# Kernel tuning notes

Hardware: AMD Instinct MI355X
Metric: run time of the kernel (lower is better)

## Reference

```python
import jax, jax.numpy as jnp
import numpy as np

B, N = 2, 65536
C_DIM, HID, OUT_DIM = 128, 32, 1
Z = Y = X = 64
SLOPE = 0.01  # torch default leaky_relu negative slope
TOTAL_PARAMS = 3 * HID + HID + HID * HID + HID + HID * OUT_DIM + OUT_DIM  # 1217


def leaky(x):
    return jnp.where(x >= 0, x, SLOPE * x)


def sample_grid_feature(c, p):
    """Trilinear grid_sample, align_corners=True, border padding.
    c: [B, C, Z, Y, X]; p: [B, N, 3] with (x, y, z) voxel coords -> [B, N, C]."""
    Bc, C, Zc, Yc, Xc = c.shape
    cb = jnp.moveaxis(c, 1, -1)  # [B, Z, Y, X, C]

    def src_index(v, S):
        # normalize_gridcloud -> clamp(-2,2) -> grid_sample unnormalize -> border clip
        g = jnp.clip(2.0 * v / (S - 1) - 1.0, -2.0, 2.0)
        ix = (g + 1.0) * 0.5 * (S - 1)
        return jnp.clip(ix, 0.0, S - 1)  # border padding clips the coordinate

    ix = src_index(p[..., 0], Xc)
    iy = src_index(p[..., 1], Yc)
    iz = src_index(p[..., 2], Zc)

    x0 = jnp.floor(ix); y0 = jnp.floor(iy); z0 = jnp.floor(iz)
    wx = ix - x0; wy = iy - y0; wz = iz - z0
    x0i = jnp.clip(x0.astype(jnp.int32), 0, Xc - 1); x1i = jnp.clip(x0i + 1, 0, Xc - 1)
    y0i = jnp.clip(y0.astype(jnp.int32), 0, Yc - 1); y1i = jnp.clip(y0i + 1, 0, Yc - 1)
    z0i = jnp.clip(z0.astype(jnp.int32), 0, Zc - 1); z1i = jnp.clip(z0i + 1, 0, Zc - 1)

    bidx = jnp.arange(Bc)[:, None]  # [B,1] broadcasts with [B,N] indices

    def g(zi, yi, xi):
        return cb[bidx, zi, yi, xi]  # [B, N, C]

    wx = wx[..., None]; wy = wy[..., None]; wz = wz[..., None]
    c00 = g(z0i, y0i, x0i) * (1 - wx) + g(z0i, y0i, x1i) * wx
    c01 = g(z0i, y1i, x0i) * (1 - wx) + g(z0i, y1i, x1i) * wx
    c10 = g(z1i, y0i, x0i) * (1 - wx) + g(z1i, y0i, x1i) * wx
    c11 = g(z1i, y1i, x0i) * (1 - wx) + g(z1i, y1i, x1i) * wx
    c0 = c00 * (1 - wy) + c01 * wy
    c1 = c10 * (1 - wy) + c11 * wy
    return c0 * (1 - wz) + c1 * wz


def setup_inputs() -> dict:
    key = jax.random.key(0)
    ks = jax.random.split(key, 8)
    pcl = jax.random.normal(ks[0], (B, N, 3), dtype=jnp.float32)
    pcl_mem = jax.random.uniform(ks[1], (B, N, 3), dtype=jnp.float32,
                                 minval=0.0, maxval=float(X - 1))
    c_plane = jax.random.normal(ks[2], (B, C_DIM, Z, Y, X), dtype=jnp.float32) * 0.1
    std = 0.21  # weights_init
    Wh1 = jax.random.normal(ks[3], (C_DIM, HID), dtype=jnp.float32) * std
    bh1 = jnp.zeros((HID,), jnp.float32)
    Wh2 = jax.random.normal(ks[4], (HID, HID), dtype=jnp.float32) * std
    bh2 = jnp.zeros((HID,), jnp.float32)
    Wh3 = jax.random.normal(ks[5], (HID, TOTAL_PARAMS), dtype=jnp.float32) * std
    bh3 = jnp.zeros((TOTAL_PARAMS,), jnp.float32)
    return {"pcl": pcl, "pcl_mem": pcl_mem, "c_plane": c_plane,
            "Wh1": Wh1, "bh1": bh1, "Wh2": Wh2, "bh2": bh2, "Wh3": Wh3, "bh3": bh3}


def reference(pcl, pcl_mem, c_plane, Wh1, bh1, Wh2, bh2, Wh3, bh3):
    feats = sample_grid_feature(c_plane, pcl_mem)  # [B, N, c_dim]
    # hypernet MLP producing per-point dynamic weights
    h = leaky(feats @ Wh1 + bh1)
    h = leaky(h @ Wh2 + bh2)
    hw = h @ Wh3 + bh3  # [B, N, 1217]

    p = 0
    W1 = hw[..., p:p + 3 * HID].reshape(B, N, 3, HID); p += 3 * HID
    b1 = hw[..., p:p + HID]; p += HID
    W2 = hw[..., p:p + HID * HID].reshape(B, N, HID, HID); p += HID * HID
    b2 = hw[..., p:p + HID]; p += HID
    W3 = hw[..., p:p + HID * OUT_DIM].reshape(B, N, HID, OUT_DIM); p += HID * OUT_DIM
    b3 = hw[..., p:p + OUT_DIM]

    # hyp.use_delta_mem_coords: fractional offset within voxel, centered
    x = pcl_mem - jnp.trunc(pcl_mem) - 0.5  # [B, N, 3]

    o = jnp.einsum('bni,bnio->bno', x, W1) + b1
    o = jnp.einsum('bni,bnio->bno', leaky(o), W2) + b2
    o = jnp.einsum('bni,bnio->bno', leaky(o), W3) + b3  # [B, N, 1]
    out = o[..., 0]  # squeeze(-1)
    return (out, feats)
```

## Files before the change

kernel.cpp:

```cpp
#include <hip/hip_runtime.h>
#include <cstdint>

#define NB 2
#define NPER 65536
#define NPTS (NB*NPER)
#define CDIM 128
#define SV 64
#define VOX (SV*SV*SV)
#define WCOLS 1217
#define WSTRIDE 1232

typedef float f2 __attribute__((ext_vector_type(2)));

__device__ __forceinline__ f2 mk2(float a, float b){ f2 r; r.x=a; r.y=b; return r; }
__device__ __forceinline__ f2 pkfma(f2 a, f2 b, f2 c){
#if __has_builtin(__builtin_elementwise_fma)
    return __builtin_elementwise_fma(a, b, c);
#else
    f2 r; r.x = fmaf(a.x, b.x, c.x); r.y = fmaf(a.y, b.y, c.y); return r;
#endif
}

__global__ __launch_bounds__(256) void transpose_kernel(const float* __restrict__ in,
                                                        float* __restrict__ out){
    __shared__ float tile[128][33];
    const int blk = blockIdx.x;
    const int b  = blk >> 13;
    const int v0 = (blk & 8191) << 5;
    const int tx = threadIdx.x & 31;
    const int ty = threadIdx.x >> 5;
    const float* ip = in + (size_t)b*128*VOX + v0;
    #pragma unroll
    for (int cc = 0; cc < 16; cc++){
        int c = cc*8 + ty;
        tile[c][tx] = ip[(size_t)c*VOX + tx];
    }
    __syncthreads();
    const int cx = threadIdx.x & 127;
    const int vy = threadIdx.x >> 7;
    float* op = out + ((size_t)b*VOX + v0)*128;
    #pragma unroll
    for (int vv = 0; vv < 16; vv++){
        int v = vv*2 + vy;
        op[(size_t)v*128 + cx] = tile[cx][v];
    }
}

__global__ __launch_bounds__(256) void sample_kernel(const float* __restrict__ pcl_mem,
                                                     const float* __restrict__ ct,
                                                     float* __restrict__ feats){
    const int tid  = threadIdx.x;
    const int lane = tid & 63;
    const int p    = blockIdx.x*4 + (tid >> 6);
    const int b    = p >> 16;

    float v0 = pcl_mem[3*p+0], v1 = pcl_mem[3*p+1], v2 = pcl_mem[3*p+2];
    auto src = [](float v){
        float g = 2.0f*v/63.0f - 1.0f;
        g = fminf(fmaxf(g, -2.0f), 2.0f);
        float t = (g + 1.0f)*0.5f*63.0f;
        return fminf(fmaxf(t, 0.0f), 63.0f);
    };
    float ix = src(v0), iy = src(v1), iz = src(v2);
    float fx = floorf(ix), fy = floorf(iy), fz = floorf(iz);
    float wx = ix-fx, wy = iy-fy, wz = iz-fz;
    int x0 = min(max((int)fx,0),63); int x1 = min(x0+1,63);
    int y0 = min(max((int)fy,0),63); int y1 = min(y0+1,63);
    int z0 = min(max((int)fz,0),63); int z1 = min(z0+1,63);
    float wx0 = 1.f-wx, wy0 = 1.f-wy, wz0 = 1.f-wz;

    const float2* base = (const float2*)ct + (size_t)b*VOX*64 + lane;
    float ax = 0.f, ay = 0.f;
#define CORNER(zz,yy,xx,wgt) { \
        float2 cv = base[(size_t)(((zz)*64+(yy))*64+(xx))*64]; \
        float w_ = (wgt); \
        ax = fmaf(w_, cv.x, ax); ay = fmaf(w_, cv.y, ay); }
    CORNER(z0,y0,x0, wz0*wy0*wx0);
    CORNER(z0,y0,x1, wz0*wy0*wx );
    CORNER(z0,y1,x0, wz0*wy *wx0);
    CORNER(z0,y1,x1, wz0*wy *wx );
    CORNER(z1,y0,x0, wz *wy0*wx0);
    CORNER(z1,y0,x1, wz *wy0*wx );
    CORNER(z1,y1,x0, wz *wy *wx0);
    CORNER(z1,y1,x1, wz *wy *wx );
#undef CORNER
    ((float2*)(feats + (size_t)p*CDIM))[lane] = make_float2(ax, ay);
}

__global__ __launch_bounds__(256) void sample_slow_kernel(const float* __restrict__ pcl_mem,
                                                          const float* __restrict__ cpl,
                                                          float* __restrict__ feats){
    int gid = blockIdx.x*256 + threadIdx.x;
    int p = gid >> 7; int c = gid & 127;
    int b = p >> 16;
    float v0 = pcl_mem[3*p+0], v1 = pcl_mem[3*p+1], v2 = pcl_mem[3*p+2];
    auto src = [](float v){
        float g = 2.0f*v/63.0f - 1.0f;
        g = fminf(fmaxf(g, -2.0f), 2.0f);
        float t = (g + 1.0f)*0.5f*63.0f;
        return fminf(fmaxf(t, 0.0f), 63.0f);
    };
    float ix = src(v0), iy = src(v1), iz = src(v2);
    float fx = floorf(ix), fy = floorf(iy), fz = floorf(iz);
    float wx = ix-fx, wy = iy-fy, wz = iz-fz;
    int x0 = min(max((int)fx,0),63); int x1 = min(x0+1,63);
    int y0 = min(max((int)fy,0),63); int y1 = min(y0+1,63);
    int z0 = min(max((int)fz,0),63); int z1 = min(z0+1,63);
    float wx0 = 1.f-wx, wy0 = 1.f-wy, wz0 = 1.f-wz;
    const float* base = cpl + ((size_t)(b*128 + c))*VOX;
    float acc = 0.f;
    acc = fmaf(wz0*wy0*wx0, base[(z0*64+y0)*64+x0], acc);
    acc = fmaf(wz0*wy0*wx , base[(z0*64+y0)*64+x1], acc);
    acc = fmaf(wz0*wy *wx0, base[(z0*64+y1)*64+x0], acc);
    acc = fmaf(wz0*wy *wx , base[(z0*64+y1)*64+x1], acc);
    acc = fmaf(wz *wy0*wx0, base[(z1*64+y0)*64+x0], acc);
    acc = fmaf(wz *wy0*wx , base[(z1*64+y0)*64+x1], acc);
    acc = fmaf(wz *wy *wx0, base[(z1*64+y1)*64+x0], acc);
    acc = fmaf(wz *wy *wx , base[(z1*64+y1)*64+x1], acc);
    feats[gid] = acc;
}

__global__ __launch_bounds__(512) void mlp_kernel(
        const float* __restrict__ pcl_mem,
        const float* __restrict__ Wh1, const float* __restrict__ bh1,
        const float* __restrict__ Wh2, const float* __restrict__ bh2,
        const float* __restrict__ Wh3, const float* __restrict__ bh3,
        const float* __restrict__ feats,
        float* __restrict__ outp)
{
    __shared__ __align__(16) float W3s[32*WSTRIDE];
    const int tid = threadIdx.x;
    const int p   = blockIdx.x*512 + tid;

    for (int t = tid; t < 32*WCOLS; t += 512){
        int k = t / WCOLS;
        int c = t - k*WCOLS;
        W3s[k*WSTRIDE + c] = Wh3[t];
    }
    __syncthreads();

    float xv0, xv1, xv2;
    {
        float v0 = pcl_mem[3*p+0], v1 = pcl_mem[3*p+1], v2 = pcl_mem[3*p+2];
        xv0 = v0 - truncf(v0) - 0.5f;
        xv1 = v1 - truncf(v1) - 0.5f;
        xv2 = v2 - truncf(v2) - 0.5f;
    }

    const float4* f4  = (const float4*)(feats + (size_t)p*CDIM);
    const float4* W1q = (const float4*)Wh1;
    const float4* W2q = (const float4*)Wh2;
    const float4* b1q = (const float4*)bh1;
    const float4* b2q = (const float4*)bh2;
    const float4* b3q = (const float4*)bh3;

    f2 h1v[16];
    #pragma unroll
    for (int jv=0;jv<8;jv++){ float4 bv=b1q[jv]; h1v[2*jv]=mk2(bv.x,bv.y); h1v[2*jv+1]=mk2(bv.z,bv.w); }
    for (int c4=0;c4<32;c4++){
        float4 f = f4[c4];
        float fs[4] = {f.x, f.y, f.z, f.w};
        #pragma unroll
        for (int cc=0;cc<4;cc++){
            f2 fc = mk2(fs[cc], fs[cc]);
            #pragma unroll
            for (int jv=0;jv<8;jv++){
                float4 w = W1q[(c4*4+cc)*8 + jv];
                h1v[2*jv]   = pkfma(fc, mk2(w.x,w.y), h1v[2*jv]);
                h1v[2*jv+1] = pkfma(fc, mk2(w.z,w.w), h1v[2*jv+1]);
            }
        }
    }
    float ha[32];
    #pragma unroll
    for (int t=0;t<16;t++){
        float a0=h1v[t].x, a1=h1v[t].y;
        ha[2*t]   = fmaxf(a0, 0.01f*a0);
        ha[2*t+1] = fmaxf(a1, 0.01f*a1);
    }

    f2 h2v[16];
    #pragma unroll
    for (int kv=0;kv<8;kv++){ float4 bv=b2q[kv]; h2v[2*kv]=mk2(bv.x,bv.y); h2v[2*kv+1]=mk2(bv.z,bv.w); }
    #pragma unroll
    for (int j=0;j<32;j++){
        f2 aj = mk2(ha[j], ha[j]);
        #pragma unroll
        for (int kv=0;kv<8;kv++){
            float4 w = W2q[j*8+kv];
            h2v[2*kv]   = pkfma(aj, mk2(w.x,w.y), h2v[2*kv]);
            h2v[2*kv+1] = pkfma(aj, mk2(w.z,w.w), h2v[2*kv+1]);
        }
    }
    float h2a[32];
    #pragma unroll
    for (int t=0;t<16;t++){
        float a0=h2v[t].x, a1=h2v[t].y;
        h2a[2*t]   = fmaxf(a0, 0.01f*a0);
        h2a[2*t+1] = fmaxf(a1, 0.01f*a1);
    }

    const f2 x0 = mk2(xv0,xv0), x1 = mk2(xv1,xv1), x2 = mk2(xv2,xv2);

    float a1r[32];
    #pragma unroll
    for (int jc=0;jc<4;jc++){
        f2 accv[4];
        #pragma unroll
        for (int q=0;q<2;q++){
            float4 ba=b3q[jc*2+q], bb=b3q[8+jc*2+q], bc=b3q[16+jc*2+q], bd=b3q[24+jc*2+q];
            accv[2*q]   = pkfma(x0,mk2(ba.x,ba.y), pkfma(x1,mk2(bb.x,bb.y), pkfma(x2,mk2(bc.x,bc.y), mk2(bd.x,bd.y))));
            accv[2*q+1] = pkfma(x0,mk2(ba.z,ba.w), pkfma(x1,mk2(bb.z,bb.w), pkfma(x2,mk2(bc.z,bc.w), mk2(bd.z,bd.w))));
        }
        #pragma unroll
        for (int k=0;k<32;k++){
            const float4* row = (const float4*)(W3s + k*WSTRIDE) + jc*2;
            f2 hk = mk2(h2a[k], h2a[k]);
            #pragma unroll
            for (int q=0;q<2;q++){
                float4 wa=row[q], wb=row[8+q], wc=row[16+q], wd=row[24+q];
                f2 m0 = pkfma(x0,mk2(wa.x,wa.y), pkfma(x1,mk2(wb.x,wb.y), pkfma(x2,mk2(wc.x,wc.y), mk2(wd.x,wd.y))));
                f2 m1 = pkfma(x0,mk2(wa.z,wa.w), pkfma(x1,mk2(wb.z,wb.w), pkfma(x2,mk2(wc.z,wc.w), mk2(wd.z,wd.w))));
                accv[2*q]   = pkfma(hk, m0, accv[2*q]);
                accv[2*q+1] = pkfma(hk, m1, accv[2*q+1]);
            }
        }
        #pragma unroll
        for (int q=0;q<2;q++){
            float a0=accv[2*q].x, a1=accv[2*q].y, a2=accv[2*q+1].x, a3=accv[2*q+1].y;
            a1r[jc*8+4*q+0] = fmaxf(a0, 0.01f*a0);
            a1r[jc*8+4*q+1] = fmaxf(a1, 0.01f*a1);
            a1r[jc*8+4*q+2] = fmaxf(a2, 0.01f*a2);
            a1r[jc*8+4*q+3] = fmaxf(a3, 0.01f*a3);
        }
    }

    f2 o2v[16];
    #pragma unroll
    for (int jv=0;jv<8;jv++){ float4 bv=b3q[288+jv]; o2v[2*jv]=mk2(bv.x,bv.y); o2v[2*jv+1]=mk2(bv.z,bv.w); }
    #pragma unroll
    for (int k=0;k<32;k++){
        const float4* row = (const float4*)(W3s + k*WSTRIDE) + 288;
        f2 hk = mk2(h2a[k], h2a[k]);
        #pragma unroll
        for (int jv=0;jv<8;jv++){
            float4 w = row[jv];
            o2v[2*jv]   = pkfma(hk, mk2(w.x,w.y), o2v[2*jv]);
            o2v[2*jv+1] = pkfma(hk, mk2(w.z,w.w), o2v[2*jv+1]);
        }
    }

    #pragma unroll 1
    for (int i=0;i<32;i++){
        f2 ai = mk2(a1r[0], a1r[0]);
        f2 w2v[16];
        #pragma unroll
        for (int jv=0;jv<8;jv++){ float4 bv=b3q[32+i*8+jv]; w2v[2*jv]=mk2(bv.x,bv.y); w2v[2*jv+1]=mk2(bv.z,bv.w); }
        #pragma unroll
        for (int k=0;k<32;k++){
            const float4* row = (const float4*)(W3s + k*WSTRIDE) + 32 + i*8;
            f2 hk = mk2(h2a[k], h2a[k]);
            #pragma unroll
            for (int jv=0;jv<8;jv++){
                float4 w = row[jv];
                w2v[2*jv]   = pkfma(hk, mk2(w.x,w.y), w2v[2*jv]);
                w2v[2*jv+1] = pkfma(hk, mk2(w.z,w.w), w2v[2*jv+1]);
            }
        }
        #pragma unroll
        for (int t=0;t<16;t++) o2v[t] = pkfma(ai, w2v[t], o2v[t]);
        #pragma unroll
        for (int t=0;t<31;t++) a1r[t] = a1r[t+1];
    }

    float a2r[32];
    #pragma unroll
    for (int t=0;t<16;t++){
        float a0=o2v[t].x, a1=o2v[t].y;
        a2r[2*t]   = fmaxf(a0, 0.01f*a0);
        a2r[2*t+1] = fmaxf(a1, 0.01f*a1);
    }

    float o3 = bh3[1216];
    #pragma unroll
    for (int k=0;k<32;k++) o3 = fmaf(h2a[k], W3s[k*WSTRIDE + 1216], o3);
    #pragma unroll
    for (int jc=0;jc<4;jc++){
        float w3c[8];
        #pragma unroll
        for (int q=0;q<2;q++){
            float4 bv=b3q[296+jc*2+q];
            w3c[4*q]=bv.x; w3c[4*q+1]=bv.y; w3c[4*q+2]=bv.z; w3c[4*q+3]=bv.w;
        }
        #pragma unroll
        for (int k=0;k<32;k++){
            const float4* row = (const float4*)(W3s + k*WSTRIDE) + 296 + jc*2;
            float hk = h2a[k];
            #pragma unroll
            for (int q=0;q<2;q++){
                float4 w=row[q];
                w3c[4*q+0] = fmaf(hk, w.x, w3c[4*q+0]);
                w3c[4*q+1] = fmaf(hk, w.y, w3c[4*q+1]);
                w3c[4*q+2] = fmaf(hk, w.z, w3c[4*q+2]);
                w3c[4*q+3] = fmaf(hk, w.w, w3c[4*q+3]);
            }
        }
        #pragma unroll
        for (int r=0;r<8;r++) o3 = fmaf(a2r[jc*8+r], w3c[r], o3);
    }

    outp[p] = o3;
}

extern "C" void kernel_launch(void* const* d_in, const int* in_sizes, int n_in,
                              void* d_out, int out_size, void* d_ws, size_t ws_size,
                              hipStream_t stream)
{
    const float* pcl_mem = (const float*)d_in[1];
    const float* c_plane = (const float*)d_in[2];
    const float* Wh1     = (const float*)d_in[3];
    const float* bh1     = (const float*)d_in[4];
    const float* Wh2     = (const float*)d_in[5];
    const float* bh2     = (const float*)d_in[6];
    const float* Wh3     = (const float*)d_in[7];
    const float* bh3     = (const float*)d_in[8];
    float* outp  = (float*)d_out;
    float* feats = outp + NPTS;

    const size_t ct_bytes = (size_t)NB*VOX*CDIM*sizeof(float);
    if (ws_size >= ct_bytes) {
        float* ct = (float*)d_ws;
        transpose_kernel<<<NB*(VOX/32), 256, 0, stream>>>(c_plane, ct);
        sample_kernel<<<NPTS/4, 256, 0, stream>>>(pcl_mem, ct, feats);
    } else {
        sample_slow_kernel<<<(NPTS*CDIM)/256, 256, 0, stream>>>(pcl_mem, c_plane, feats);
    }

    mlp_kernel<<<NPTS/512, 512, 0, stream>>>(pcl_mem, Wh1, bh1, Wh2, bh2, Wh3, bh3, feats, outp);
}
```

Before: 715.8 us.

## Process two points per thread in MLP kernel to reuse shared-memory weight loads

Each thread of the MLP kernel now computes two points, so each shared-memory read of the hypernet output weights feeds two sets of FMAs. The block shrinks to 256 threads with the same 512 points per block, and the W2-generation loop is split into column chunks to limit live registers. This targets LDS bandwidth as the limit in the per-point dynamic-weight stage. In exchange it roughly doubles register pressure and halves the threads per block, which may lower occupancy or cause spills.

```diff
diff --git a/kernel.cpp b/kernel.cpp
--- a/kernel.cpp
+++ b/kernel.cpp
@@ -120,7 +120,7 @@
     feats[gid] = acc;
 }
 
-__global__ __launch_bounds__(512) void mlp_kernel(
+__global__ __launch_bounds__(256, 1) void mlp_kernel(
         const float* __restrict__ pcl_mem,
         const float* __restrict__ Wh1, const float* __restrict__ bh1,
         const float* __restrict__ Wh2, const float* __restrict__ bh2,
@@ -130,186 +130,255 @@
 {
     __shared__ __align__(16) float W3s[32*WSTRIDE];
     const int tid = threadIdx.x;
-    const int p   = blockIdx.x*512 + tid;
-
-    for (int t = tid; t < 32*WCOLS; t += 512){
+    const int pA  = blockIdx.x*512 + tid;
+    const int pB  = pA + 256;
+
+    for (int t = tid; t < 32*WCOLS; t += 256){
         int k = t / WCOLS;
         int c = t - k*WCOLS;
         W3s[k*WSTRIDE + c] = Wh3[t];
     }
     __syncthreads();
 
-    float xv0, xv1, xv2;
+    float xA0, xA1, xA2, xB0, xB1, xB2;
     {
-        float v0 = pcl_mem[3*p+0], v1 = pcl_mem[3*p+1], v2 = pcl_mem[3*p+2];
-        xv0 = v0 - truncf(v0) - 0.5f;
-        xv1 = v1 - truncf(v1) - 0.5f;
-        xv2 = v2 - truncf(v2) - 0.5f;
-    }
-
-    const float4* f4  = (const float4*)(feats + (size_t)p*CDIM);
+        float v0 = pcl_mem[3*pA+0], v1 = pcl_mem[3*pA+1], v2 = pcl_mem[3*pA+2];
+        xA0 = v0 - truncf(v0) - 0.5f; xA1 = v1 - truncf(v1) - 0.5f; xA2 = v2 - truncf(v2) - 0.5f;
+        float u0 = pcl_mem[3*pB+0], u1 = pcl_mem[3*pB+1], u2 = pcl_mem[3*pB+2];
+        xB0 = u0 - truncf(u0) - 0.5f; xB1 = u1 - truncf(u1) - 0.5f; xB2 = u2 - truncf(u2) - 0.5f;
+    }
+
+    const float4* f4A = (const float4*)(feats + (size_t)pA*CDIM);
+    const float4* f4B = (const float4*)(feats + (size_t)pB*CDIM);
     const float4* W1q = (const float4*)Wh1;
     const float4* W2q = (const float4*)Wh2;
     const float4* b1q = (const float4*)bh1;
     const float4* b2q = (const float4*)bh2;
     const float4* b3q = (const float4*)bh3;
 
-    f2 h1v[16];
-    #pragma unroll
-    for (int jv=0;jv<8;jv++){ float4 bv=b1q[jv]; h1v[2*jv]=mk2(bv.x,bv.y); h1v[2*jv+1]=mk2(bv.z,bv.w); }
+    f2 h1A[16], h1B[16];
+    #pragma unroll
+    for (int jv=0;jv<8;jv++){
+        float4 bv=b1q[jv];
+        h1A[2*jv]=mk2(bv.x,bv.y); h1A[2*jv+1]=mk2(bv.z,bv.w);
+        h1B[2*jv]=mk2(bv.x,bv.y); h1B[2*jv+1]=mk2(bv.z,bv.w);
+    }
     for (int c4=0;c4<32;c4++){
-        float4 f = f4[c4];
-        float fs[4] = {f.x, f.y, f.z, f.w};
+        float4 fa = f4A[c4], fb = f4B[c4];
+        float fsA[4] = {fa.x, fa.y, fa.z, fa.w};
+        float fsB[4] = {fb.x, fb.y, fb.z, fb.w};
         #pragma unroll
         for (int cc=0;cc<4;cc++){
-            f2 fc = mk2(fs[cc], fs[cc]);
+            f2 fcA = mk2(fsA[cc], fsA[cc]);
+            f2 fcB = mk2(fsB[cc], fsB[cc]);
             #pragma unroll
             for (int jv=0;jv<8;jv++){
                 float4 w = W1q[(c4*4+cc)*8 + jv];
-                h1v[2*jv]   = pkfma(fc, mk2(w.x,w.y), h1v[2*jv]);
-                h1v[2*jv+1] = pkfma(fc, mk2(w.z,w.w), h1v[2*jv+1]);
-            }
-        }
-    }
-    float ha[32];
+                f2 wlo = mk2(w.x,w.y), whi = mk2(w.z,w.w);
+                h1A[2*jv]   = pkfma(fcA, wlo, h1A[2*jv]);
+                h1A[2*jv+1] = pkfma(fcA, whi, h1A[2*jv+1]);
+                h1B[2*jv]   = pkfma(fcB, wlo, h1B[2*jv]);
+                h1B[2*jv+1] = pkfma(fcB, whi, h1B[2*jv+1]);
+            }
+        }
+    }
+    float haA[32], haB[32];
     #pragma unroll
     for (int t=0;t<16;t++){
-        float a0=h1v[t].x, a1=h1v[t].y;
-        ha[2*t]   = fmaxf(a0, 0.01f*a0);
-        ha[2*t+1] = fmaxf(a1, 0.01f*a1);
-    }
-
-    f2 h2v[16];
-    #pragma unroll
-    for (int kv=0;kv<8;kv++){ float4 bv=b2q[kv]; h2v[2*kv]=mk2(bv.x,bv.y); h2v[2*kv+1]=mk2(bv.z,bv.w); }
+        float a0=h1A[t].x, a1=h1A[t].y, b0=h1B[t].x, b1=h1B[t].y;
+        haA[2*t]=fmaxf(a0,0.01f*a0); haA[2*t+1]=fmaxf(a1,0.01f*a1);
+        haB[2*t]=fmaxf(b0,0.01f*b0); haB[2*t+1]=fmaxf(b1,0.01f*b1);
+    }
+
+    f2 h2A[16], h2B[16];
+    #pragma unroll
+    for (int kv=0;kv<8;kv++){
+        float4 bv=b2q[kv];
+        h2A[2*kv]=mk2(bv.x,bv.y); h2A[2*kv+1]=mk2(bv.z,bv.w);
+        h2B[2*kv]=mk2(bv.x,bv.y); h2B[2*kv+1]=mk2(bv.z,bv.w);
+    }
     #pragma unroll
     for (int j=0;j<32;j++){
-        f2 aj = mk2(ha[j], ha[j]);
+        f2 ajA = mk2(haA[j], haA[j]);
+        f2 ajB = mk2(haB[j], haB[j]);
         #pragma unroll
         for (int kv=0;kv<8;kv++){
             float4 w = W2q[j*8+kv];
-            h2v[2*kv]   = pkfma(aj, mk2(w.x,w.y), h2v[2*kv]);
-            h2v[2*kv+1] = pkfma(aj, mk2(w.z,w.w), h2v[2*kv+1]);
-        }
-    }
-    float h2a[32];
+            f2 wlo = mk2(w.x,w.y), whi = mk2(w.z,w.w);
+            h2A[2*kv]   = pkfma(ajA, wlo, h2A[2*kv]);
+            h2A[2*kv+1] = pkfma(ajA, whi, h2A[2*kv+1]);
+            h2B[2*kv]   = pkfma(ajB, wlo, h2B[2*kv]);
+            h2B[2*kv+1] = pkfma(ajB, whi, h2B[2*kv+1]);
+        }
+    }
+    float h2aA[32], h2aB[32];
     #pragma unroll
     for (int t=0;t<16;t++){
-        float a0=h2v[t].x, a1=h2v[t].y;
-        h2a[2*t]   = fmaxf(a0, 0.01f*a0);
-        h2a[2*t+1] = fmaxf(a1, 0.01f*a1);
-    }
-
-    const f2 x0 = mk2(xv0,xv0), x1 = mk2(xv1,xv1), x2 = mk2(xv2,xv2);
-
-    float a1r[32];
+        float a0=h2A[t].x, a1=h2A[t].y, b0=h2B[t].x, b1=h2B[t].y;
+        h2aA[2*t]=fmaxf(a0,0.01f*a0); h2aA[2*t+1]=fmaxf(a1,0.01f*a1);
+        h2aB[2*t]=fmaxf(b0,0.01f*b0); h2aB[2*t+1]=fmaxf(b1,0.01f*b1);
+    }
+
+    const f2 xa0=mk2(xA0,xA0), xa1=mk2(xA1,xA1), xa2=mk2(xA2,xA2);
+    const f2 xb0=mk2(xB0,xB0), xb1=mk2(xB1,xB1), xb2=mk2(xB2,xB2);
+
+    float a1A[32], a1B[32];
     #pragma unroll
     for (int jc=0;jc<4;jc++){
-        f2 accv[4];
+        f2 accA[4], accB[4];
         #pragma unroll
         for (int q=0;q<2;q++){
             float4 ba=b3q[jc*2+q], bb=b3q[8+jc*2+q], bc=b3q[16+jc*2+q], bd=b3q[24+jc*2+q];
-            accv[2*q]   = pkfma(x0,mk2(ba.x,ba.y), pkfma(x1,mk2(bb.x,bb.y), pkfma(x2,mk2(bc.x,bc.y), mk2(bd.x,bd.y))));
-            accv[2*q+1] = pkfma(x0,mk2(ba.z,ba.w), pkfma(x1,mk2(bb.z,bb.w), pkfma(x2,mk2(bc.z,bc.w), mk2(bd.z,bd.w))));
+            f2 balo=mk2(ba.x,ba.y), bahi=mk2(ba.z,ba.w);
+            f2 bblo=mk2(bb.x,bb.y), bbhi=mk2(bb.z,bb.w);
+            f2 bclo=mk2(bc.x,bc.y), bchi=mk2(bc.z,bc.w);
+            f2 bdlo=mk2(bd.x,bd.y), bdhi=mk2(bd.z,bd.w);
+            accA[2*q]   = pkfma(xa0,balo, pkfma(xa1,bblo, pkfma(xa2,bclo, bdlo)));
+            accA[2*q+1] = pkfma(xa0,bahi, pkfma(xa1,bbhi, pkfma(xa2,bchi, bdhi)));
+            accB[2*q]   = pkfma(xb0,balo, pkfma(xb1,bblo, pkfma(xb2,bclo, bdlo)));
+            accB[2*q+1] = pkfma(xb0,bahi, pkfma(xb1,bbhi, pkfma(xb2,bchi, bdhi)));
         }
         #pragma unroll
         for (int k=0;k<32;k++){
             const float4* row = (const float4*)(W3s + k*WSTRIDE) + jc*2;
-            f2 hk = mk2(h2a[k], h2a[k]);
+            f2 hkA = mk2(h2aA[k], h2aA[k]);
+            f2 hkB = mk2(h2aB[k], h2aB[k]);
             #pragma unroll
             for (int q=0;q<2;q++){
                 float4 wa=row[q], wb=row[8+q], wc=row[16+q], wd=row[24+q];
-                f2 m0 = pkfma(x0,mk2(wa.x,wa.y), pkfma(x1,mk2(wb.x,wb.y), pkfma(x2,mk2(wc.x,wc.y), mk2(wd.x,wd.y))));
-                f2 m1 = pkfma(x0,mk2(wa.z,wa.w), pkfma(x1,mk2(wb.z,wb.w), pkfma(x2,mk2(wc.z,wc.w), mk2(wd.z,wd.w))));
-                accv[2*q]   = pkfma(hk, m0, accv[2*q]);
-                accv[2*q+1] = pkfma(hk, m1, accv[2*q+1]);
+                f2 walo=mk2(wa.x,wa.y), wahi=mk2(wa.z,wa.w);
+                f2 wblo=mk2(wb.x,wb.y), wbhi=mk2(wb.z,wb.w);
+                f2 wclo=mk2(wc.x,wc.y), wchi=mk2(wc.z,wc.w);
+                f2 wdlo=mk2(wd.x,wd.y), wdhi=mk2(wd.z,wd.w);
+                f2 mA0 = pkfma(xa0,walo, pkfma(xa1,wblo, pkfma(xa2,wclo, wdlo)));
+                f2 mA1 = pkfma(xa0,wahi, pkfma(xa1,wbhi, pkfma(xa2,wchi, wdhi)));
+                f2 mB0 = pkfma(xb0,walo, pkfma(xb1,wblo, pkfma(xb2,wclo, wdlo)));
+                f2 mB1 = pkfma(xb0,wahi, pkfma(xb1,wbhi, pkfma(xb2,wchi, wdhi)));
+                accA[2*q]   = pkfma(hkA, mA0, accA[2*q]);
+                accA[2*q+1] = pkfma(hkA, mA1, accA[2*q+1]);
+                accB[2*q]   = pkfma(hkB, mB0, accB[2*q]);
+                accB[2*q+1] = pkfma(hkB, mB1, accB[2*q+1]);
             }
         }
         #pragma unroll
         for (int q=0;q<2;q++){
-            float a0=accv[2*q].x, a1=accv[2*q].y, a2=accv[2*q+1].x, a3=accv[2*q+1].y;
-            a1r[jc*8+4*q+0] = fmaxf(a0, 0.01f*a0);
-            a1r[jc*8+4*q+1] = fmaxf(a1, 0.01f*a1);
-            a1r[jc*8+4*q+2] = fmaxf(a2, 0.01f*a2);
-            a1r[jc*8+4*q+3] = fmaxf(a3, 0.01f*a3);
-        }
-    }
-
-    f2 o2v[16];
-    #pragma unroll
-    for (int jv=0;jv<8;jv++){ float4 bv=b3q[288+jv]; o2v[2*jv]=mk2(bv.x,bv.y); o2v[2*jv+1]=mk2(bv.z,bv.w); }
+            float a0=accA[2*q].x, a1=accA[2*q].y, a2=accA[2*q+1].x, a3=accA[2*q+1].y;
+            a1A[jc*8+4*q+0]=fmaxf(a0,0.01f*a0); a1A[jc*8+4*q+1]=fmaxf(a1,0.01f*a1);
+            a1A[jc*8+4*q+2]=fmaxf(a2,0.01f*a2); a1A[jc*8+4*q+3]=fmaxf(a3,0.01f*a3);
+            float b0=accB[2*q].x, b1=accB[2*q].y, b2=accB[2*q+1].x, b3=accB[2*q+1].y;
+            a1B[jc*8+4*q+0]=fmaxf(b0,0.01f*b0); a1B[jc*8+4*q+1]=fmaxf(b1,0.01f*b1);
+            a1B[jc*8+4*q+2]=fmaxf(b2,0.01f*b2); a1B[jc*8+4*q+3]=fmaxf(b3,0.01f*b3);
+        }
+    }
+
+    f2 o2A[16], o2B[16];
+    #pragma unroll
+    for (int jv=0;jv<8;jv++){
+        float4 bv=b3q[288+jv];
+        o2A[2*jv]=mk2(bv.x,bv.y); o2A[2*jv+1]=mk2(bv.z,bv.w);
+        o2B[2*jv]=mk2(bv.x,bv.y); o2B[2*jv+1]=mk2(bv.z,bv.w);
+    }
     #pragma unroll
     for (int k=0;k<32;k++){
         const float4* row = (const float4*)(W3s + k*WSTRIDE) + 288;
-        f2 hk = mk2(h2a[k], h2a[k]);
+        f2 hkA = mk2(h2aA[k], h2aA[k]);
+        f2 hkB = mk2(h2aB[k], h2aB[k]);
         #pragma unroll
         for (int jv=0;jv<8;jv++){
             float4 w = row[jv];
-            o2v[2*jv]   = pkfma(hk, mk2(w.x,w.y), o2v[2*jv]);
-            o2v[2*jv+1] = pkfma(hk, mk2(w.z,w.w), o2v[2*jv+1]);
+            f2 wlo = mk2(w.x,w.y), whi = mk2(w.z,w.w);
+            o2A[2*jv]   = pkfma(hkA, wlo, o2A[2*jv]);
+            o2A[2*jv+1] = pkfma(hkA, whi, o2A[2*jv+1]);
+            o2B[2*jv]   = pkfma(hkB, wlo, o2B[2*jv]);
+            o2B[2*jv+1] = pkfma(hkB, whi, o2B[2*jv+1]);
         }
     }
 
     #pragma unroll 1
     for (int i=0;i<32;i++){
-        f2 ai = mk2(a1r[0], a1r[0]);
-        f2 w2v[16];
-        #pragma unroll
-        for (int jv=0;jv<8;jv++){ float4 bv=b3q[32+i*8+jv]; w2v[2*jv]=mk2(bv.x,bv.y); w2v[2*jv+1]=mk2(bv.z,bv.w); }
-        #pragma unroll
-        for (int k=0;k<32;k++){
-            const float4* row = (const float4*)(W3s + k*WSTRIDE) + 32 + i*8;
-            f2 hk = mk2(h2a[k], h2a[k]);
-            #pragma unroll
-            for (int jv=0;jv<8;jv++){
-                float4 w = row[jv];
-                w2v[2*jv]   = pkfma(hk, mk2(w.x,w.y), w2v[2*jv]);
-                w2v[2*jv+1] = pkfma(hk, mk2(w.z,w.w), w2v[2*jv+1]);
-            }
-        }
-        #pragma unroll
-        for (int t=0;t<16;t++) o2v[t] = pkfma(ai, w2v[t], o2v[t]);
-        #pragma unroll
-        for (int t=0;t<31;t++) a1r[t] = a1r[t+1];
-    }
-
-    float a2r[32];
+        f2 aiA = mk2(a1A[0], a1A[0]);
+        f2 aiB = mk2(a1B[0], a1B[0]);
+        #pragma unroll
+        for (int jc=0;jc<4;jc++){
+            f2 w2A[4], w2B[4];
+            #pragma unroll
+            for (int q=0;q<2;q++){
+                float4 bv=b3q[32+i*8+jc*2+q];
+                f2 blo=mk2(bv.x,bv.y), bhi=mk2(bv.z,bv.w);
+                w2A[2*q]=blo; w2A[2*q+1]=bhi;
+                w2B[2*q]=blo; w2B[2*q+1]=bhi;
+            }
+            #pragma unroll
+            for (int k=0;k<32;k++){
+                const float4* row = (const float4*)(W3s + k*WSTRIDE) + 32 + i*8 + jc*2;
+                f2 hkA = mk2(h2aA[k], h2aA[k]);
+                f2 hkB = mk2(h2aB[k], h2aB[k]);
+                #pragma unroll
+                for (int q=0;q<2;q++){
+                    float4 w = row[q];
+                    f2 wlo = mk2(w.x,w.y), whi = mk2(w.z,w.w);
+                    w2A[2*q]   = pkfma(hkA, wlo, w2A[2*q]);
+                    w2A[2*q+1] = pkfma(hkA, whi, w2A[2*q+1]);
+                    w2B[2*q]   = pkfma(hkB, wlo, w2B[2*q]);
+                    w2B[2*q+1] = pkfma(hkB, whi, w2B[2*q+1]);
+                }
+            }
+            #pragma unroll
+            for (int t=0;t<4;t++){
+                o2A[jc*4+t] = pkfma(aiA, w2A[t], o2A[jc*4+t]);
+                o2B[jc*4+t] = pkfma(aiB, w2B[t], o2B[jc*4+t]);
+            }
+        }
+        #pragma unroll
+        for (int t=0;t<31;t++){ a1A[t]=a1A[t+1]; a1B[t]=a1B[t+1]; }
+    }
+
+    float a2A[32], a2B[32];
     #pragma unroll
     for (int t=0;t<16;t++){
-        float a0=o2v[t].x, a1=o2v[t].y;
-        a2r[2*t]   = fmaxf(a0, 0.01f*a0);
-        a2r[2*t+1] = fmaxf(a1, 0.01f*a1);
-    }
-
-    float o3 = bh3[1216];
-    #pragma unroll
-    for (int k=0;k<32;k++) o3 = fmaf(h2a[k], W3s[k*WSTRIDE + 1216], o3);
+        float a0=o2A[t].x, a1=o2A[t].y, b0=o2B[t].x, b1=o2B[t].y;
+        a2A[2*t]=fmaxf(a0,0.01f*a0); a2A[2*t+1]=fmaxf(a1,0.01f*a1);
+        a2B[2*t]=fmaxf(b0,0.01f*b0); a2B[2*t+1]=fmaxf(b1,0.01f*b1);
+    }
+
+    float o3A = bh3[1216], o3B = bh3[1216];
+    #pragma unroll
+    for (int k=0;k<32;k++){
+        float w = W3s[k*WSTRIDE + 1216];
+        o3A = fmaf(h2aA[k], w, o3A);
+        o3B = fmaf(h2aB[k], w, o3B);
+    }
     #pragma unroll
     for (int jc=0;jc<4;jc++){
-        float w3c[8];
+        float w3A[8], w3B[8];
         #pragma unroll
         for (int q=0;q<2;q++){
             float4 bv=b3q[296+jc*2+q];
-            w3c[4*q]=bv.x; w3c[4*q+1]=bv.y; w3c[4*q+2]=bv.z; w3c[4*q+3]=bv.w;
+            w3A[4*q]=bv.x; w3A[4*q+1]=bv.y; w3A[4*q+2]=bv.z; w3A[4*q+3]=bv.w;
+            w3B[4*q]=bv.x; w3B[4*q+1]=bv.y; w3B[4*q+2]=bv.z; w3B[4*q+3]=bv.w;
         }
         #pragma unroll
         for (int k=0;k<32;k++){
             const float4* row = (const float4*)(W3s + k*WSTRIDE) + 296 + jc*2;
-            float hk = h2a[k];
+            float hkA = h2aA[k], hkB = h2aB[k];
             #pragma unroll
             for (int q=0;q<2;q++){
                 float4 w=row[q];
-                w3c[4*q+0] = fmaf(hk, w.x, w3c[4*q+0]);
-                w3c[4*q+1] = fmaf(hk, w.y, w3c[4*q+1]);
-                w3c[4*q+2] = fmaf(hk, w.z, w3c[4*q+2]);
-                w3c[4*q+3] = fmaf(hk, w.w, w3c[4*q+3]);
-            }
-        }
-        #pragma unroll
-        for (int r=0;r<8;r++) o3 = fmaf(a2r[jc*8+r], w3c[r], o3);
-    }
-
-    outp[p] = o3;
+                w3A[4*q+0]=fmaf(hkA,w.x,w3A[4*q+0]); w3A[4*q+1]=fmaf(hkA,w.y,w3A[4*q+1]);
+                w3A[4*q+2]=fmaf(hkA,w.z,w3A[4*q+2]); w3A[4*q+3]=fmaf(hkA,w.w,w3A[4*q+3]);
+                w3B[4*q+0]=fmaf(hkB,w.x,w3B[4*q+0]); w3B[4*q+1]=fmaf(hkB,w.y,w3B[4*q+1]);
+                w3B[4*q+2]=fmaf(hkB,w.z,w3B[4*q+2]); w3B[4*q+3]=fmaf(hkB,w.w,w3B[4*q+3]);
+            }
+        }
+        #pragma unroll
+        for (int r=0;r<8;r++){
+            o3A = fmaf(a2A[jc*8+r], w3A[r], o3A);
+            o3B = fmaf(a2B[jc*8+r], w3B[r], o3B);
+        }
+    }
+
+    outp[pA] = o3A;
+    outp[pB] = o3B;
 }
 
 extern "C" void kernel_launch(void* const* d_in, const int* in_sizes, int n_in,
@@ -336,5 +405,5 @@
         sample_slow_kernel<<<(NPTS*CDIM)/256, 256, 0, stream>>>(pcl_mem, c_plane, feats);
     }
 
-    mlp_kernel<<<NPTS/512, 512, 0, stream>>>(pcl_mem, Wh1, bh1, Wh2, bh2, Wh3, bh3, feats, outp);
-}
+    mlp_kernel<<<NPTS/512, 256, 0, stream>>>(pcl_mem, Wh1, bh1, Wh2, bh2, Wh3, bh3, feats, outp);
+}
```

After: 903.1 us. +26.2%, slower.
